# Optimization experiments

Measured on AMD Instinct MI355X. Metric: run time of the kernel, lower is better.

The kernel has to match this reference:

```python
import jax, jax.numpy as jnp
import numpy as np

N, E, IN, OUT, R, B = 50000, 800000, 16, 16, 90, 30


def setup_inputs() -> dict:
    key = jax.random.key(0)
    ks = jax.random.split(key, 9)
    h = jax.random.normal(ks[0], (N, IN), dtype=jnp.float32)
    he = jax.random.normal(ks[1], (E, IN), dtype=jnp.float32)
    Ws = jax.random.normal(ks[2], (OUT, IN), dtype=jnp.float32) * 0.1      # shared_weight.weight
    Wa = jax.random.normal(ks[3], (1, 3 * OUT), dtype=jnp.float32) * 0.1   # attn_fc.weight
    weight = jax.random.normal(ks[4], (B, IN, OUT), dtype=jnp.float32) * 0.1  # basis weights
    w_comp = jax.random.normal(ks[5], (R, B), dtype=jnp.float32) * 0.1        # basis coefficients
    src = jax.random.randint(ks[6], (E,), 0, N)
    dst = jax.random.randint(ks[7], (E,), 0, N)
    rel_type = jax.random.randint(ks[8], (E,), 0, R)
    return {"h": h, "he": he, "Ws": Ws, "Wa": Wa, "weight": weight,
            "w_comp": w_comp, "src": src, "dst": dst, "rel_type": rel_type}


def reference(h, he, Ws, Wa, weight, w_comp, src, dst, rel_type):
    n_nodes, in_dim = h.shape
    num_bases, _, out_dim = weight.shape
    num_rels = w_comp.shape[0]

    # Basis decomposition, replicating the original's reshape semantics exactly:
    # view [B,in,out] -> [in,B,out], matmul with w_comp [R,B] -> [in,R,out], view -> [R,in,out]
    V = weight.reshape(in_dim, num_bases, out_dim)
    W_rel = jnp.matmul(w_comp, V).reshape(num_rels, in_dim, out_dim)  # [R,in,out]

    # edge_attention: GAT-like score from concat(z_src, z_edge, z_dst)
    h_src = h[src]                      # [E,in]
    z_src = h_src @ Ws.T                # [E,out]
    z_dst = h[dst] @ Ws.T               # [E,out]
    z_e = he @ Ws.T                     # [E,out]
    e = jnp.concatenate([z_src, z_e, z_dst], axis=1) @ Wa.T  # [E,1] (no leaky_relu / no softmax in original)

    # message: per-edge relation-specific bmm, scaled by attention score
    msg = jnp.einsum('ei,eio->eo', h_src, W_rel[rel_type]) * e  # [E,out]

    # reduce: scatter-sum into destination nodes (bias=None, activation=None)
    h_out = jax.ops.segment_sum(msg, dst, num_segments=n_nodes)  # [N,out]
    return h_out
```

## Files before the change

kernel.cpp:

```cpp
#include <hip/hip_runtime.h>

#define N_NODES 50000
#define N_EDGES 800000
#define IN_DIM 16
#define OUT_DIM 16
#define N_RELS 90
#define N_BASES 30

#define CAP 24
#define LDS_STRIDE 260
#define EDGES_PER_BLK 3125

#define PREP_BLOCKS 91
#define DOTS_BLOCKS 196
#define ZERO_BLOCKS 196
#define HZ_BLOCKS 782

__device__ __forceinline__ float4 shfl_xor4(float4 v, int m) {
    float4 r;
    r.x = __shfl_xor(v.x, m); r.y = __shfl_xor(v.y, m);
    r.z = __shfl_xor(v.z, m); r.w = __shfl_xor(v.w, m);
    return r;
}

__global__ __launch_bounds__(256) void setup_kernel(
    const float* __restrict__ Ws,
    const float* __restrict__ Wa,
    const float* __restrict__ weight,
    const float* __restrict__ w_comp,
    const float* __restrict__ h,
    float* __restrict__ Wrel,
    float* __restrict__ avec,
    float2* __restrict__ s13,
    int* __restrict__ cnt,
    float* __restrict__ hout)
{
    int b = blockIdx.x;
    if (b < PREP_BLOCKS) {
        int f = b * 256 + threadIdx.x;
        if (f < N_RELS * IN_DIM * OUT_DIM) {
            int a   = f / (N_RELS * OUT_DIM);
            int rem = f % (N_RELS * OUT_DIM);
            int r   = rem / OUT_DIM;
            int o   = rem % OUT_DIM;
            float acc = 0.f;
            #pragma unroll
            for (int bb = 0; bb < N_BASES; ++bb)
                acc += w_comp[r * N_BASES + bb] * weight[a * (N_BASES * OUT_DIM) + bb * OUT_DIM + o];
            Wrel[f] = acc;
        } else if (f < N_RELS * IN_DIM * OUT_DIM + 48) {
            int g = f - N_RELS * IN_DIM * OUT_DIM;
            int k = g / IN_DIM;
            int i = g % IN_DIM;
            float acc = 0.f;
            #pragma unroll
            for (int o = 0; o < OUT_DIM; ++o)
                acc += Wa[k * OUT_DIM + o] * Ws[o * IN_DIM + i];
            avec[g] = acc;
        }
    } else if (b < PREP_BLOCKS + DOTS_BLOCKS) {
        __shared__ float la[48];
        if (threadIdx.x < 48) {
            int k = threadIdx.x / IN_DIM;
            int i = threadIdx.x % IN_DIM;
            float acc = 0.f;
            #pragma unroll
            for (int o = 0; o < OUT_DIM; ++o)
                acc += Wa[k * OUT_DIM + o] * Ws[o * IN_DIM + i];
            la[threadIdx.x] = acc;
        }
        __syncthreads();
        int n = (b - PREP_BLOCKS) * 256 + threadIdx.x;
        if (n >= N_NODES) return;
        const float4* p = (const float4*)(h + (size_t)n * IN_DIM);
        float d1 = 0.f, d3 = 0.f;
        #pragma unroll
        for (int i = 0; i < 4; ++i) {
            float4 v = p[i];
            d1 += v.x * la[4*i+0] + v.y * la[4*i+1] + v.z * la[4*i+2] + v.w * la[4*i+3];
            d3 += v.x * la[32+4*i+0] + v.y * la[32+4*i+1] + v.z * la[32+4*i+2] + v.w * la[32+4*i+3];
        }
        s13[n] = make_float2(d1, d3);
    } else if (b < PREP_BLOCKS + DOTS_BLOCKS + ZERO_BLOCKS) {
        int n = (b - PREP_BLOCKS - DOTS_BLOCKS) * 256 + threadIdx.x;
        if (n < N_NODES) cnt[n] = 0;
    } else {
        int idx = (b - PREP_BLOCKS - DOTS_BLOCKS - ZERO_BLOCKS) * 256 + threadIdx.x;
        if (idx < N_NODES * OUT_DIM / 4) {
            float4 z = {0.f, 0.f, 0.f, 0.f};
            ((float4*)hout)[idx] = z;
        }
    }
}

__global__ __launch_bounds__(1024) void compute_lds_kernel(
    const float* __restrict__ h,
    const float* __restrict__ he,
    const int* __restrict__ src,
    const int* __restrict__ dst,
    const int* __restrict__ rel,
    const float* __restrict__ Wrel,
    const float* __restrict__ avec,
    const float2* __restrict__ s13,
    int* __restrict__ cnt,
    float* __restrict__ bucket,
    float* __restrict__ hout)
{
    extern __shared__ float lw[];

    for (int j = threadIdx.x; j < N_RELS * 64; j += 1024) {
        int r = j >> 6;
        int w = j & 63;
        float4 v = ((const float4*)Wrel)[r * 64 + w];
        *(float4*)(lw + r * LDS_STRIDE + w * 4) = v;
    }
    __syncthreads();

    const int t = threadIdx.x;
    const int q = t & 3;
    const int grp = t >> 2;
    const int lbase = (t & 63) & ~3;
    const int ebeg = blockIdx.x * EDGES_PER_BLK;
    const int eend = ebeg + EDGES_PER_BLK;

    float4 av = *(const float4*)(avec + 16 + 4 * q);

    for (int base = ebeg + grp; base < eend; base += 1024) {
        int e[4], s[4], d[4], r[4];
        bool val[4];

        #pragma unroll
        for (int k = 0; k < 4; ++k) {
            e[k] = base + k * 256;
            val[k] = (e[k] < eend);
            int ec = val[k] ? e[k] : ebeg;
            s[k] = src[ec]; d[k] = dst[ec]; r[k] = rel[ec];
        }

        float4 heq[4], hq[4];
        float2 svs[4], svd[4];
        #pragma unroll
        for (int k = 0; k < 4; ++k) {
            int ec = val[k] ? e[k] : ebeg;
            heq[k] = *(const float4*)(he + (size_t)ec * IN_DIM + q * 4);
            hq[k]  = *(const float4*)(h  + (size_t)s[k] * IN_DIM + q * 4);
            svs[k] = s13[s[k]];
            svd[k] = s13[d[k]];
        }

        int slot[4];
        #pragma unroll
        for (int k = 0; k < 4; ++k) {
            slot[k] = 0;
            if (q == 0 && val[k]) slot[k] = atomicAdd(&cnt[d[k]], 1);
        }

        #pragma unroll
        for (int k = 0; k < 4; ++k) {
            if (!val[k]) continue;
            int sl = __shfl(slot[k], lbase);

            float pd = heq[k].x * av.x + heq[k].y * av.y + heq[k].z * av.z + heq[k].w * av.w;
            pd += __shfl_xor(pd, 1);
            pd += __shfl_xor(pd, 2);
            float score = svs[k].x + svd[k].y + pd;

            float4 o1 = shfl_xor4(hq[k], 1);
            float4 o2 = shfl_xor4(hq[k], 2);
            float4 o3 = shfl_xor4(o1, 2);
            bool q0 = (q == 0), q1 = (q == 1), q2 = (q == 2);
            float4 row0 = q0 ? hq[k] : q1 ? o1 : q2 ? o2 : o3;
            float4 row1 = q0 ? o1 : q1 ? hq[k] : q2 ? o3 : o2;
            float4 row2 = q0 ? o2 : q1 ? o3 : q2 ? hq[k] : o1;
            float4 row3 = q0 ? o3 : q1 ? o2 : q2 ? o1 : hq[k];
            float hs[16] = {row0.x,row0.y,row0.z,row0.w, row1.x,row1.y,row1.z,row1.w,
                            row2.x,row2.y,row2.z,row2.w, row3.x,row3.y,row3.z,row3.w};

            const float* wb = lw + (size_t)r[k] * LDS_STRIDE + q * 4;
            float4 acc = {0.f, 0.f, 0.f, 0.f};
            #pragma unroll
            for (int i = 0; i < 16; ++i) {
                float4 w = *(const float4*)(wb + i * 16);
                float hv = hs[i];
                acc.x += hv * w.x; acc.y += hv * w.y; acc.z += hv * w.z; acc.w += hv * w.w;
            }
            acc.x *= score; acc.y *= score; acc.z *= score; acc.w *= score;

            if (sl < CAP) {
                *(float4*)(bucket + ((size_t)d[k] * CAP + sl) * OUT_DIM + q * 4) = acc;
            } else {
                float* outp = hout + (size_t)d[k] * OUT_DIM + q * 4;
                atomicAdd(outp + 0, acc.x);
                atomicAdd(outp + 1, acc.y);
                atomicAdd(outp + 2, acc.z);
                atomicAdd(outp + 3, acc.w);
            }
        }
    }
}

__global__ __launch_bounds__(256) void reduce_bucket_kernel(
    const float* __restrict__ bucket,
    const int* __restrict__ cnt,
    float* __restrict__ hout)
{
    int tid = blockIdx.x * 256 + threadIdx.x;
    int n = tid >> 4;
    int l = tid & 15;
    int q = l & 3;
    int p = l >> 2;
    if (n >= N_NODES) return;

    int deg = cnt[n];
    int m = deg > CAP ? CAP : deg;
    const float4* bp = (const float4*)(bucket + (size_t)n * CAP * OUT_DIM) + q;
    float4 acc = {0.f, 0.f, 0.f, 0.f};
    for (int j = p; j < m; j += 4) {
        float4 v = bp[j * 4];
        acc.x += v.x; acc.y += v.y; acc.z += v.z; acc.w += v.w;
    }
    acc.x += __shfl_xor(acc.x, 4); acc.y += __shfl_xor(acc.y, 4);
    acc.z += __shfl_xor(acc.z, 4); acc.w += __shfl_xor(acc.w, 4);
    acc.x += __shfl_xor(acc.x, 8); acc.y += __shfl_xor(acc.y, 8);
    acc.z += __shfl_xor(acc.z, 8); acc.w += __shfl_xor(acc.w, 8);

    if (p == 0) {
        if (deg <= CAP) {
            *(float4*)(hout + (size_t)n * OUT_DIM + q * 4) = acc;
        } else {
            float* outp = hout + (size_t)n * OUT_DIM + q * 4;
            atomicAdd(outp + 0, acc.x);
            atomicAdd(outp + 1, acc.y);
            atomicAdd(outp + 2, acc.z);
            atomicAdd(outp + 3, acc.w);
        }
    }
}

__global__ __launch_bounds__(256) void prep_kernel(
    const float* __restrict__ Ws, const float* __restrict__ Wa,
    const float* __restrict__ weight, const float* __restrict__ w_comp,
    float* __restrict__ Wrel, float* __restrict__ avec)
{
    int f = blockIdx.x * blockDim.x + threadIdx.x;
    if (f < N_RELS * IN_DIM * OUT_DIM) {
        int a   = f / (N_RELS * OUT_DIM);
        int rem = f % (N_RELS * OUT_DIM);
        int r   = rem / OUT_DIM;
        int o   = rem % OUT_DIM;
        float acc = 0.f;
        #pragma unroll
        for (int b = 0; b < N_BASES; ++b)
            acc += w_comp[r * N_BASES + b] * weight[a * (N_BASES * OUT_DIM) + b * OUT_DIM + o];
        Wrel[f] = acc;
    } else if (f < N_RELS * IN_DIM * OUT_DIM + 48) {
        int g = f - N_RELS * IN_DIM * OUT_DIM;
        int k = g / IN_DIM;
        int i = g % IN_DIM;
        float acc = 0.f;
        #pragma unroll
        for (int o = 0; o < OUT_DIM; ++o)
            acc += Wa[k * OUT_DIM + o] * Ws[o * IN_DIM + i];
        avec[g] = acc;
    }
}

__global__ __launch_bounds__(256) void edge_atomic_kernel(
    const float* __restrict__ h,
    const float* __restrict__ he,
    const int* __restrict__ src,
    const int* __restrict__ dst,
    const int* __restrict__ rel,
    const float* __restrict__ Wrel,
    const float* __restrict__ avec,
    float* __restrict__ hout)
{
    int e = blockIdx.x * blockDim.x + threadIdx.x;
    if (e >= N_EDGES) return;
    int s = src[e], d = dst[e], r = rel[e];
    float hs[IN_DIM];
    const float4* p = (const float4*)(h + (size_t)s * IN_DIM);
    #pragma unroll
    for (int i = 0; i < 4; ++i) {
        float4 v = p[i];
        hs[4*i+0] = v.x; hs[4*i+1] = v.y; hs[4*i+2] = v.z; hs[4*i+3] = v.w;
    }
    float score = 0.f;
    #pragma unroll
    for (int i = 0; i < IN_DIM; ++i) score += hs[i] * avec[i];
    const float4* qe = (const float4*)(he + (size_t)e * IN_DIM);
    #pragma unroll
    for (int i = 0; i < 4; ++i) {
        float4 v = qe[i];
        score += v.x * avec[16+4*i] + v.y * avec[17+4*i] + v.z * avec[18+4*i] + v.w * avec[19+4*i];
    }
    const float4* pd = (const float4*)(h + (size_t)d * IN_DIM);
    #pragma unroll
    for (int i = 0; i < 4; ++i) {
        float4 v = pd[i];
        score += v.x * avec[32+4*i] + v.y * avec[33+4*i] + v.z * avec[34+4*i] + v.w * avec[35+4*i];
    }
    float acc[OUT_DIM];
    #pragma unroll
    for (int o = 0; o < OUT_DIM; ++o) acc[o] = 0.f;
    const float* W = Wrel + (size_t)r * 256;
    #pragma unroll
    for (int i = 0; i < IN_DIM; ++i) {
        float hv = hs[i];
        #pragma unroll
        for (int o = 0; o < OUT_DIM; ++o) acc[o] += hv * W[i * OUT_DIM + o];
    }
    float* outp = hout + (size_t)d * OUT_DIM;
    #pragma unroll
    for (int o = 0; o < OUT_DIM; ++o) atomicAdd(outp + o, acc[o] * score);
}

extern "C" void kernel_launch(void* const* d_in, const int* in_sizes, int n_in,
                              void* d_out, int out_size, void* d_ws, size_t ws_size,
                              hipStream_t stream) {
    const float* h      = (const float*)d_in[0];
    const float* he     = (const float*)d_in[1];
    const float* Ws     = (const float*)d_in[2];
    const float* Wa     = (const float*)d_in[3];
    const float* weight = (const float*)d_in[4];
    const float* w_comp = (const float*)d_in[5];
    const int*   src    = (const int*)d_in[6];
    const int*   dst    = (const int*)d_in[7];
    const int*   rel    = (const int*)d_in[8];
    float* hout = (float*)d_out;

    const size_t OFF_WREL   = 0;
    const size_t OFF_AVEC   = 23040;
    const size_t OFF_S13    = 23104;
    const size_t OFF_CNT    = 123104;
    const size_t OFF_BUCKET = 173104;
    const size_t NEED_BUCKET = (OFF_BUCKET + (size_t)N_NODES * CAP * OUT_DIM) * 4;

    float* wsf  = (float*)d_ws;
    float* Wrel = wsf + OFF_WREL;
    float* avec = wsf + OFF_AVEC;
    float2* s13 = (float2*)(wsf + OFF_S13);
    int* cnt    = (int*)(wsf + OFF_CNT);

    if (ws_size >= NEED_BUCKET) {
        float* bucket = wsf + OFF_BUCKET;

        setup_kernel<<<PREP_BLOCKS + DOTS_BLOCKS + ZERO_BLOCKS + HZ_BLOCKS, 256, 0, stream>>>(
            Ws, Wa, weight, w_comp, h, Wrel, avec, s13, cnt, hout);
        compute_lds_kernel<<<N_EDGES / EDGES_PER_BLK, 1024,
                             N_RELS * LDS_STRIDE * sizeof(float), stream>>>(
            h, he, src, dst, rel, Wrel, avec, s13, cnt, bucket, hout);
        reduce_bucket_kernel<<<(N_NODES * 16 + 255) / 256, 256, 0, stream>>>(
            bucket, cnt, hout);
    } else {
        hipMemsetAsync(d_out, 0, (size_t)out_size * sizeof(float), stream);
        int total = N_RELS * IN_DIM * OUT_DIM + 48;
        prep_kernel<<<(total + 255) / 256, 256, 0, stream>>>(Ws, Wa, weight, w_comp, Wrel, avec);
        edge_atomic_kernel<<<(N_EDGES + 255) / 256, 256, 0, stream>>>(
            h, he, src, dst, rel, Wrel, avec, hout);
    }
}
```

Before: 188.3 us.

## Bucket compact edge descriptors and defer per-edge bmm to reduce kernel

The edge pass now computes only the attention score and writes a compact 8-byte entry (packed src/rel plus score) into per-destination buckets, instead of a full 64-byte message. The relation-specific matvec moves into the per-node reduce kernel, which loads Wrel into LDS and accumulates scaled messages directly, removing the large intermediate write and read of messages. Bucket capacity rises so fewer edges spill to atomics. The cost is that the reduce kernel now gathers h rows per edge, and its work is uneven because node degrees vary, which can leave some lanes idle.

```diff
diff --git a/kernel.cpp b/kernel.cpp
--- a/kernel.cpp
+++ b/kernel.cpp
@@ -7,14 +7,15 @@
 #define N_RELS 90
 #define N_BASES 30
 
-#define CAP 24
+#define CAP 64
 #define LDS_STRIDE 260
-#define EDGES_PER_BLK 3125
 
 #define PREP_BLOCKS 91
 #define DOTS_BLOCKS 196
 #define ZERO_BLOCKS 196
 #define HZ_BLOCKS 782
+
+#define NODES_PER_RBLK 256
 
 __device__ __forceinline__ float4 shfl_xor4(float4 v, int m) {
     float4 r;
@@ -93,7 +94,7 @@
     }
 }
 
-__global__ __launch_bounds__(1024) void compute_lds_kernel(
+__global__ __launch_bounds__(256) void route_kernel(
     const float* __restrict__ h,
     const float* __restrict__ he,
     const int* __restrict__ src,
@@ -103,11 +104,60 @@
     const float* __restrict__ avec,
     const float2* __restrict__ s13,
     int* __restrict__ cnt,
-    float* __restrict__ bucket,
+    uint2* __restrict__ bucket,
     float* __restrict__ hout)
 {
+    int e = blockIdx.x * 256 + threadIdx.x;
+    if (e >= N_EDGES) return;
+    int s = src[e], d = dst[e], r = rel[e];
+
+    const float4* hep = (const float4*)(he + (size_t)e * IN_DIM);
+    const float4* ap  = (const float4*)(avec + 16);
+    float pd = 0.f;
+    #pragma unroll
+    for (int i = 0; i < 4; ++i) {
+        float4 v = hep[i];
+        float4 a = ap[i];
+        pd += v.x * a.x + v.y * a.y + v.z * a.z + v.w * a.w;
+    }
+    float2 ss = s13[s];
+    float2 sd = s13[d];
+    float score = ss.x + sd.y + pd;
+
+    int slot = atomicAdd(&cnt[d], 1);
+    if (slot < CAP) {
+        uint2 ent;
+        ent.x = ((unsigned)r << 16) | (unsigned)s;
+        ent.y = __float_as_uint(score);
+        bucket[(size_t)d * CAP + slot] = ent;
+    } else {
+        float hs[16];
+        const float4* hp = (const float4*)(h + (size_t)s * IN_DIM);
+        #pragma unroll
+        for (int i = 0; i < 4; ++i) {
+            float4 v = hp[i];
+            hs[4*i+0] = v.x; hs[4*i+1] = v.y; hs[4*i+2] = v.z; hs[4*i+3] = v.w;
+        }
+        const float* W = Wrel + (size_t)r * 256;
+        float* outp = hout + (size_t)d * OUT_DIM;
+        #pragma unroll
+        for (int o = 0; o < OUT_DIM; ++o) {
+            float acc = 0.f;
+            #pragma unroll
+            for (int i = 0; i < IN_DIM; ++i) acc += hs[i] * W[i * OUT_DIM + o];
+            atomicAdd(outp + o, acc * score);
+        }
+    }
+}
+
+__global__ __launch_bounds__(1024) void reduce_bmm_kernel(
+    const float* __restrict__ h,
+    const float* __restrict__ Wrel,
+    const uint2* __restrict__ bucket,
+    const int* __restrict__ cnt,
+    float* __restrict__ hout)
+{
     extern __shared__ float lw[];
-
     for (int j = threadIdx.x; j < N_RELS * 64; j += 1024) {
         int r = j >> 6;
         int w = j & 63;
@@ -116,54 +166,39 @@
     }
     __syncthreads();
 
-    const int t = threadIdx.x;
-    const int q = t & 3;
-    const int grp = t >> 2;
-    const int lbase = (t & 63) & ~3;
-    const int ebeg = blockIdx.x * EDGES_PER_BLK;
-    const int eend = ebeg + EDGES_PER_BLK;
-
-    float4 av = *(const float4*)(avec + 16 + 4 * q);
-
-    for (int base = ebeg + grp; base < eend; base += 1024) {
-        int e[4], s[4], d[4], r[4];
+    int n = blockIdx.x * NODES_PER_RBLK + (threadIdx.x >> 2);
+    int q = threadIdx.x & 3;
+    if (n >= N_NODES) return;
+
+    int deg = cnt[n];
+    int m = deg > CAP ? CAP : deg;
+    const uint2* ep = bucket + (size_t)n * CAP;
+    float4 acc = {0.f, 0.f, 0.f, 0.f};
+
+    for (int j0 = 0; j0 < m; j0 += 4) {
+        uint2 ent[4];
+        float4 hq[4];
         bool val[4];
 
         #pragma unroll
         for (int k = 0; k < 4; ++k) {
-            e[k] = base + k * 256;
-            val[k] = (e[k] < eend);
-            int ec = val[k] ? e[k] : ebeg;
-            s[k] = src[ec]; d[k] = dst[ec]; r[k] = rel[ec];
-        }
-
-        float4 heq[4], hq[4];
-        float2 svs[4], svd[4];
+            int j = j0 + k;
+            val[k] = (j < m);
+            int jc = j < m ? j : (m - 1);
+            ent[k] = ep[jc];
+        }
+
         #pragma unroll
         for (int k = 0; k < 4; ++k) {
-            int ec = val[k] ? e[k] : ebeg;
-            heq[k] = *(const float4*)(he + (size_t)ec * IN_DIM + q * 4);
-            hq[k]  = *(const float4*)(h  + (size_t)s[k] * IN_DIM + q * 4);
-            svs[k] = s13[s[k]];
-            svd[k] = s13[d[k]];
-        }
-
-        int slot[4];
-        #pragma unroll
-        for (int k = 0; k < 4; ++k) {
-            slot[k] = 0;
-            if (q == 0 && val[k]) slot[k] = atomicAdd(&cnt[d[k]], 1);
+            int s = ent[k].x & 0xFFFF;
+            hq[k] = *(const float4*)(h + (size_t)s * IN_DIM + q * 4);
         }
 
         #pragma unroll
         for (int k = 0; k < 4; ++k) {
             if (!val[k]) continue;
-            int sl = __shfl(slot[k], lbase);
-
-            float pd = heq[k].x * av.x + heq[k].y * av.y + heq[k].z * av.z + heq[k].w * av.w;
-            pd += __shfl_xor(pd, 1);
-            pd += __shfl_xor(pd, 2);
-            float score = svs[k].x + svd[k].y + pd;
+            int r = ent[k].x >> 16;
+            float score = __uint_as_float(ent[k].y);
 
             float4 o1 = shfl_xor4(hq[k], 1);
             float4 o2 = shfl_xor4(hq[k], 2);
@@ -176,64 +211,27 @@
             float hs[16] = {row0.x,row0.y,row0.z,row0.w, row1.x,row1.y,row1.z,row1.w,
                             row2.x,row2.y,row2.z,row2.w, row3.x,row3.y,row3.z,row3.w};
 
-            const float* wb = lw + (size_t)r[k] * LDS_STRIDE + q * 4;
-            float4 acc = {0.f, 0.f, 0.f, 0.f};
+            const float* wb = lw + (size_t)r * LDS_STRIDE + q * 4;
+            float4 a = {0.f, 0.f, 0.f, 0.f};
             #pragma unroll
             for (int i = 0; i < 16; ++i) {
                 float4 w = *(const float4*)(wb + i * 16);
                 float hv = hs[i];
-                acc.x += hv * w.x; acc.y += hv * w.y; acc.z += hv * w.z; acc.w += hv * w.w;
+                a.x += hv * w.x; a.y += hv * w.y; a.z += hv * w.z; a.w += hv * w.w;
             }
-            acc.x *= score; acc.y *= score; acc.z *= score; acc.w *= score;
-
-            if (sl < CAP) {
-                *(float4*)(bucket + ((size_t)d[k] * CAP + sl) * OUT_DIM + q * 4) = acc;
-            } else {
-                float* outp = hout + (size_t)d[k] * OUT_DIM + q * 4;
-                atomicAdd(outp + 0, acc.x);
-                atomicAdd(outp + 1, acc.y);
-                atomicAdd(outp + 2, acc.z);
-                atomicAdd(outp + 3, acc.w);
-            }
-        }
-    }
-}
-
-__global__ __launch_bounds__(256) void reduce_bucket_kernel(
-    const float* __restrict__ bucket,
-    const int* __restrict__ cnt,
-    float* __restrict__ hout)
-{
-    int tid = blockIdx.x * 256 + threadIdx.x;
-    int n = tid >> 4;
-    int l = tid & 15;
-    int q = l & 3;
-    int p = l >> 2;
-    if (n >= N_NODES) return;
-
-    int deg = cnt[n];
-    int m = deg > CAP ? CAP : deg;
-    const float4* bp = (const float4*)(bucket + (size_t)n * CAP * OUT_DIM) + q;
-    float4 acc = {0.f, 0.f, 0.f, 0.f};
-    for (int j = p; j < m; j += 4) {
-        float4 v = bp[j * 4];
-        acc.x += v.x; acc.y += v.y; acc.z += v.z; acc.w += v.w;
-    }
-    acc.x += __shfl_xor(acc.x, 4); acc.y += __shfl_xor(acc.y, 4);
-    acc.z += __shfl_xor(acc.z, 4); acc.w += __shfl_xor(acc.w, 4);
-    acc.x += __shfl_xor(acc.x, 8); acc.y += __shfl_xor(acc.y, 8);
-    acc.z += __shfl_xor(acc.z, 8); acc.w += __shfl_xor(acc.w, 8);
-
-    if (p == 0) {
-        if (deg <= CAP) {
-            *(float4*)(hout + (size_t)n * OUT_DIM + q * 4) = acc;
-        } else {
-            float* outp = hout + (size_t)n * OUT_DIM + q * 4;
-            atomicAdd(outp + 0, acc.x);
-            atomicAdd(outp + 1, acc.y);
-            atomicAdd(outp + 2, acc.z);
-            atomicAdd(outp + 3, acc.w);
-        }
+            acc.x += score * a.x; acc.y += score * a.y;
+            acc.z += score * a.z; acc.w += score * a.w;
+        }
+    }
+
+    float* outp = hout + (size_t)n * OUT_DIM + q * 4;
+    if (deg <= CAP) {
+        *(float4*)outp = acc;
+    } else {
+        atomicAdd(outp + 0, acc.x);
+        atomicAdd(outp + 1, acc.y);
+        atomicAdd(outp + 2, acc.z);
+        atomicAdd(outp + 3, acc.w);
     }
 }
 
@@ -334,7 +332,7 @@
     const size_t OFF_S13    = 23104;
     const size_t OFF_CNT    = 123104;
     const size_t OFF_BUCKET = 173104;
-    const size_t NEED_BUCKET = (OFF_BUCKET + (size_t)N_NODES * CAP * OUT_DIM) * 4;
+    const size_t NEED_BUCKET = OFF_BUCKET * 4 + (size_t)N_NODES * CAP * sizeof(uint2);
 
     float* wsf  = (float*)d_ws;
     float* Wrel = wsf + OFF_WREL;
@@ -343,15 +341,15 @@
     int* cnt    = (int*)(wsf + OFF_CNT);
 
     if (ws_size >= NEED_BUCKET) {
-        float* bucket = wsf + OFF_BUCKET;
+        uint2* bucket = (uint2*)(wsf + OFF_BUCKET);
 
         setup_kernel<<<PREP_BLOCKS + DOTS_BLOCKS + ZERO_BLOCKS + HZ_BLOCKS, 256, 0, stream>>>(
             Ws, Wa, weight, w_comp, h, Wrel, avec, s13, cnt, hout);
-        compute_lds_kernel<<<N_EDGES / EDGES_PER_BLK, 1024,
-                             N_RELS * LDS_STRIDE * sizeof(float), stream>>>(
+        route_kernel<<<N_EDGES / 256, 256, 0, stream>>>(
             h, he, src, dst, rel, Wrel, avec, s13, cnt, bucket, hout);
-        reduce_bucket_kernel<<<(N_NODES * 16 + 255) / 256, 256, 0, stream>>>(
-            bucket, cnt, hout);
+        reduce_bmm_kernel<<<(N_NODES + NODES_PER_RBLK - 1) / NODES_PER_RBLK, 1024,
+                            N_RELS * LDS_STRIDE * sizeof(float), stream>>>(
+            h, Wrel, bucket, cnt, hout);
     } else {
         hipMemsetAsync(d_out, 0, (size_t)out_size * sizeof(float), stream);
         int total = N_RELS * IN_DIM * OUT_DIM + 48;
```

After: 187.9 us. Within noise of the previous version (-0.2%).
